# Optimization experiments

Hardware: AMD Instinct MI355X
Metric: run time of the kernel (lower is better)

Reference implementation:

```python
import jax, jax.numpy as jnp
import numpy as np

IN_DIM = 100
OUT_DIM = 200
N_ETYPES = 4
N_STEPS = 8
CONCAT = IN_DIM + OUT_DIM  # 300
EPS = 1e-5


def setup_inputs() -> dict:
    key = jax.random.key(0)
    ks = jax.random.split(key, 24)
    N, E = 100000, 1600000
    rn = lambda k, shape, s=0.05: jax.random.normal(k, shape, dtype=jnp.float32) * s
    return {
        "features": rn(ks[0], (N, IN_DIM), 1.0),
        "edge_index": jax.random.randint(ks[1], (2, E), 0, N, dtype=jnp.int32),
        "edge_types": jax.random.randint(ks[2], (E,), 0, N_ETYPES, dtype=jnp.int32),
        "ggnn_W": rn(ks[3], (N_ETYPES, OUT_DIM, OUT_DIM)),
        "ggnn_b": rn(ks[4], (N_ETYPES, OUT_DIM)),
        "gru_Wih": rn(ks[5], (3 * OUT_DIM, OUT_DIM)),
        "gru_Whh": rn(ks[6], (3 * OUT_DIM, OUT_DIM)),
        "gru_bih": rn(ks[7], (3 * OUT_DIM,)),
        "gru_bhh": rn(ks[8], (3 * OUT_DIM,)),
        "conv1_w": rn(ks[9], (OUT_DIM, OUT_DIM, 3)),
        "conv1_b": rn(ks[10], (OUT_DIM,)),
        "conv2_w": rn(ks[11], (OUT_DIM, OUT_DIM, 1)),
        "conv2_b": rn(ks[12], (OUT_DIM,)),
        "convc1_w": rn(ks[13], (CONCAT, CONCAT, 3)),
        "convc1_b": rn(ks[14], (CONCAT,)),
        "convc2_w": rn(ks[15], (CONCAT, CONCAT, 1)),
        "convc2_b": rn(ks[16], (CONCAT,)),
        "bn_y_g": jnp.ones((OUT_DIM,), jnp.float32),
        "bn_y_b": jnp.zeros((OUT_DIM,), jnp.float32),
        "bn_c_g": jnp.ones((CONCAT,), jnp.float32),
        "bn_c_b": jnp.zeros((CONCAT,), jnp.float32),
        "mlp_y_w": rn(ks[17], (2, OUT_DIM)),
        "mlp_y_b": rn(ks[18], (2,)),
        "mlp_z_w": rn(ks[19], (2, CONCAT)),
        "mlp_z_b": rn(ks[20], (2,)),
    }


def _ggnn(features, src, dst, etypes, W, b, Wih, Whh, bih, bhh):
    """DGL-style GatedGraphConv: per-etype linear, sum-aggregate, GRU update."""
    N = features.shape[0]
    h0 = jnp.concatenate(
        [features, jnp.zeros((N, OUT_DIM - IN_DIM), features.dtype)], axis=-1)

    def step(h, _):
        # transform every node by every etype weight: [n_etypes, N, OUT_DIM]
        t = jnp.einsum('koh,nh->kno', W, h) + b[:, None, :]
        msg = t[etypes, src]                         # [E, OUT_DIM] gather
        a = jax.ops.segment_sum(msg, dst, num_segments=N)  # scatter-add
        # torch GRUCell
        gi = a @ Wih.T + bih
        gh = h @ Whh.T + bhh
        ir, iz, inn = jnp.split(gi, 3, axis=-1)
        hr, hz, hn = jnp.split(gh, 3, axis=-1)
        r = jax.nn.sigmoid(ir + hr)
        z = jax.nn.sigmoid(iz + hz)
        n = jnp.tanh(inn + r * hn)
        return (1.0 - z) * n + z * h, None

    h, _ = jax.lax.scan(step, h0, None, length=N_STEPS)
    return h


def _bn(x, g, b):  # x: [1, C, L], training-mode BatchNorm1d (biased var)
    m = x.mean(axis=(0, 2), keepdims=True)
    v = x.var(axis=(0, 2), keepdims=True)
    return (x - m) * jax.lax.rsqrt(v + EPS) * g[None, :, None] + b[None, :, None]


def _conv1d(x, w, b):  # x: [N, C, L], w: [O, I, k]
    y = jax.lax.conv_general_dilated(
        x, w, window_strides=(1,), padding='VALID',
        dimension_numbers=('NCH', 'OIH', 'NCH'))
    return y + b[None, :, None]


def _maxpool1d(x, k, s):
    return jax.lax.reduce_window(x, -jnp.inf, jax.lax.max,
                                 (1, 1, k), (1, 1, s), 'VALID')


def reference(features, edge_index, edge_types, ggnn_W, ggnn_b,
              gru_Wih, gru_Whh, gru_bih, gru_bhh,
              conv1_w, conv1_b, conv2_w, conv2_b,
              convc1_w, convc1_b, convc2_w, convc2_b,
              bn_y_g, bn_y_b, bn_c_g, bn_c_b,
              mlp_y_w, mlp_y_b, mlp_z_w, mlp_z_b):
    src, dst = edge_index[0], edge_index[1]
    out = _ggnn(features, src, dst, edge_types, ggnn_W, ggnn_b,
                gru_Wih, gru_Whh, gru_bih, gru_bhh)   # [N, 200]
    x_i = features[None]            # [1, N, 100]
    h_i = out[None]                 # [1, N, 200]
    c_i = jnp.concatenate([h_i, x_i], axis=-1)  # [1, N, 300]

    y = _maxpool1d(jax.nn.relu(_bn(_conv1d(jnp.swapaxes(h_i, 1, 2), conv1_w, conv1_b), bn_y_g, bn_y_b)), 3, 2)
    Y2 = jnp.swapaxes(_maxpool1d(jax.nn.relu(_bn(_conv1d(y, conv2_w, conv2_b), bn_y_g, bn_y_b)), 2, 2), 1, 2)

    z = _maxpool1d(jax.nn.relu(_bn(_conv1d(jnp.swapaxes(c_i, 1, 2), convc1_w, convc1_b), bn_c_g, bn_c_b)), 3, 2)
    Z2 = jnp.swapaxes(_maxpool1d(jax.nn.relu(_bn(_conv1d(z, convc2_w, convc2_b), bn_c_g, bn_c_b)), 2, 2), 1, 2)

    before_avg = (Y2 @ mlp_y_w.T + mlp_y_b) * (Z2 @ mlp_z_w.T + mlp_z_b)  # [1, L, 2]
    return jax.nn.sigmoid(before_avg.mean(axis=1))  # [1, 2]
```

## Files before the change

kernel.cpp:

```cpp
#include <hip/hip_runtime.h>
#include <cstddef>
#include <cstdint>


typedef unsigned short u16;
typedef unsigned char u8;
typedef __attribute__((ext_vector_type(8))) short bf16x8;
typedef __attribute__((ext_vector_type(4))) float f32x4;
typedef __attribute__((ext_vector_type(2))) float f32x2;

static __device__ __forceinline__ float bf2f(u16 u) {
  union { unsigned int i; float f; } v; v.i = ((unsigned int)u) << 16; return v.f;
}
static __device__ __forceinline__ u16 f2bf(float f) {
  union { float f; unsigned int i; } v; v.f = f;
  unsigned int r = v.i + 0x7FFFu + ((v.i >> 16) & 1u);
  return (u16)(r >> 16);
}
static __device__ __forceinline__ float sigm(float x) { return 1.f / (1.f + __expf(-x)); }
static __device__ __forceinline__ u8 f2fp8(float x) {
  return (u8)(__builtin_amdgcn_cvt_pk_fp8_f32(x, 0.f, 0, false) & 0xff);
}

static __device__ __forceinline__ void gload16(const void* gp, void* lp) {
  __builtin_amdgcn_global_load_lds(
      (const __attribute__((address_space(1))) void*)gp,
      (__attribute__((address_space(3))) void*)lp, 16, 0, 0);
}

__global__ void fail_k(float* out, float code) { out[0] = code; out[1] = code; }

__global__ void init_hb_k(const float* __restrict__ feat, u16* __restrict__ hb, int N) {
  int total = N * 224;
  for (int i = blockIdx.x * blockDim.x + threadIdx.x; i < total; i += blockDim.x * gridDim.x) {
    int n = i / 224, c = i - n * 224;
    hb[i] = (c < 100) ? f2bf(feat[(size_t)n * 100 + c]) : (u16)0;
  }
}

__global__ void init_hq_k(const float* __restrict__ feat, u8* __restrict__ hqd,
                          u8* __restrict__ ahq, int N) {
  int total = N * 224;
  for (int i = blockIdx.x * blockDim.x + threadIdx.x; i < total; i += blockDim.x * gridDim.x) {
    int n = i / 224, c = i - n * 224;
    u8 v = (c < 100) ? f2fp8(feat[(size_t)n * 100 + c]) : (u8)0;
    hqd[i] = v;
    ahq[(size_t)n * 448 + 224 + c] = v;
  }
}

__global__ void count_deg_k(const int* __restrict__ dst, const int* __restrict__ et,
                            int* __restrict__ deg_et, int N, int E) {
  for (int e = blockIdx.x * blockDim.x + threadIdx.x; e < E; e += blockDim.x * gridDim.x)
    atomicAdd(&deg_et[et[e] * N + dst[e]], 1);
}

__global__ __launch_bounds__(1024) void bsum_k(const int* __restrict__ cnt,
                                               int* __restrict__ bsum, int L) {
  __shared__ int buf[1024];
  int i = blockIdx.x * 1024 + threadIdx.x;
  buf[threadIdx.x] = (i < L) ? cnt[i] : 0;
  __syncthreads();
  for (int o = 512; o > 0; o >>= 1) {
    if (threadIdx.x < o) buf[threadIdx.x] += buf[threadIdx.x + o];
    __syncthreads();
  }
  if (threadIdx.x == 0) bsum[blockIdx.x] = buf[0];
}

__global__ __launch_bounds__(1024) void scanb_k(int* __restrict__ bsum, int nb) {
  __shared__ int buf[1024];
  int v = (threadIdx.x < nb) ? bsum[threadIdx.x] : 0;
  buf[threadIdx.x] = v;
  __syncthreads();
  for (int o = 1; o < 1024; o <<= 1) {
    int t = (threadIdx.x >= o) ? buf[threadIdx.x - o] : 0;
    __syncthreads();
    buf[threadIdx.x] += t;
    __syncthreads();
  }
  if (threadIdx.x < nb) bsum[threadIdx.x] = buf[threadIdx.x] - v;
}

__global__ __launch_bounds__(1024) void scan_fin_k(const int* __restrict__ cnt,
                                                   const int* __restrict__ bsum,
                                                   int* __restrict__ off, int L) {
  __shared__ int buf[1024];
  int i = blockIdx.x * 1024 + threadIdx.x;
  int v = (i < L) ? cnt[i] : 0;
  buf[threadIdx.x] = v;
  __syncthreads();
  for (int o = 1; o < 1024; o <<= 1) {
    int t = (threadIdx.x >= o) ? buf[threadIdx.x - o] : 0;
    __syncthreads();
    buf[threadIdx.x] += t;
    __syncthreads();
  }
  if (i < L) off[i] = buf[threadIdx.x] - v + bsum[blockIdx.x];
}

__global__ void copy_int_k(const int* __restrict__ a, int* __restrict__ b, int n) {
  for (int i = blockIdx.x * blockDim.x + threadIdx.x; i < n; i += blockDim.x * gridDim.x) b[i] = a[i];
}

__global__ void fill_src_k(const int* __restrict__ src, const int* __restrict__ dst,
                           const int* __restrict__ et, int* __restrict__ cursor,
                           int* __restrict__ esrc, int N, int E) {
  for (int e = blockIdx.x * blockDim.x + threadIdx.x; e < E; e += blockDim.x * gridDim.x) {
    int p = atomicAdd(&cursor[et[e] * N + dst[e]], 1);
    esrc[p] = src[e];
  }
}


__global__ void pack_wcat8_k(const float* __restrict__ W, const float* __restrict__ gb,
                             u8* __restrict__ dst) {
  int total = 200 * 832;
  for (int i = blockIdx.x * blockDim.x + threadIdx.x; i < total; i += blockDim.x * gridDim.x) {
    int o = i / 832, kp = i - o * 832;
    float v = 0.f;
    if (kp < 800) { int k = kp / 200, kk = kp - k * 200; v = W[((size_t)k * 200 + o) * 200 + kk]; }
    else if (kp < 804) v = gb[(kp - 800) * 200 + o];
    dst[i] = f2fp8(v);
  }
}

__global__ void pack_wall8_k(const float* __restrict__ Wih, const float* __restrict__ Whh,
                             u8* __restrict__ dst) {
  int total = 800 * 448;
  for (int i = blockIdx.x * blockDim.x + threadIdx.x; i < total; i += blockDim.x * gridDim.x) {
    int jp = i / 448, kp = i - jp * 448;
    int o = jp >> 2, g = jp & 3;
    float v = 0.f;
    if (g == 0) {
      if (kp < 200) v = Wih[(size_t)o * 200 + kp];
      else if (kp >= 224 && kp < 424) v = Whh[(size_t)o * 200 + (kp - 224)];
    } else if (g == 1) {
      if (kp < 200) v = Wih[(size_t)(200 + o) * 200 + kp];
      else if (kp >= 224 && kp < 424) v = Whh[(size_t)(200 + o) * 200 + (kp - 224)];
    } else if (g == 2) {
      if (kp < 200) v = Wih[(size_t)(400 + o) * 200 + kp];
    } else {
      if (kp >= 224 && kp < 424) v = Whh[(size_t)(400 + o) * 200 + (kp - 224)];
    }
    dst[i] = f2fp8(v);
  }
}

__global__ void ball_i_k(const float* __restrict__ bih, const float* __restrict__ bhh,
                         float* __restrict__ ball) {
  int j = blockIdx.x * blockDim.x + threadIdx.x;
  if (j < 800) {
    int o = j >> 2, g = j & 3;
    float v;
    if (g == 0) v = bih[o] + bhh[o];
    else if (g == 1) v = bih[200 + o] + bhh[200 + o];
    else if (g == 2) v = bih[400 + o];
    else v = bhh[400 + o];
    ball[j] = v;
  }
}

__global__ void pack_lin_b(const float* __restrict__ src, u16* __restrict__ dst,
                           int Nn, int K, int Kp) {
  int total = Nn * Kp;
  for (int i = blockIdx.x * blockDim.x + threadIdx.x; i < total; i += blockDim.x * gridDim.x) {
    int o = i / Kp, kp = i - o * Kp;
    dst[i] = (kp < K) ? f2bf(src[(size_t)o * K + kp]) : (u16)0;
  }
}

__global__ void pack_w1c_k(const float* __restrict__ src, u16* __restrict__ dst) {
  int total = 200 * 1056;
  for (int i = blockIdx.x * blockDim.x + threadIdx.x; i < total; i += blockDim.x * gridDim.x) {
    int o = i / 1056, r = i - o * 1056;
    int t = r / 352, kp = r - t * 352;
    dst[i] = (kp < 200) ? f2bf(src[((size_t)o * 200 + kp) * 3 + t]) : (u16)0;
  }
}

__global__ void pack_wc1_b(const float* __restrict__ src, u16* __restrict__ dst) {
  int total = 300 * 1056;
  for (int i = blockIdx.x * blockDim.x + threadIdx.x; i < total; i += blockDim.x * gridDim.x) {
    int o = i / 1056, r = i - o * 1056;
    int t = r / 352, kp = r - t * 352;
    int ci = (kp < 224) ? (kp < 200 ? kp : -1) : ((kp - 224) < 100 ? 200 + (kp - 224) : -1);
    dst[i] = (ci >= 0) ? f2bf(src[((size_t)o * 300 + ci) * 3 + t]) : (u16)0;
  }
}

__global__ void agg8_k(const int* __restrict__ off_et, const int* __restrict__ deg_et,
                       const int* __restrict__ esrc, const u8* __restrict__ hqd,
                       u8* __restrict__ scat8, int N) {
  int gtid = blockIdx.x * blockDim.x + threadIdx.x;
  int wid = gtid >> 6, lane = threadIdx.x & 63;
  int nw = (blockDim.x * gridDim.x) >> 6;
  int sub = lane >> 4, l = lane & 15;
  for (int n = wid; n < N; n += nw) {
    u8* srow = scat8 + (size_t)n * 832;
    int rs = off_et[(size_t)sub * N + n];
    int d  = deg_et[(size_t)sub * N + n];
    f32x2 a2[8];
#pragma unroll
    for (int j = 0; j < 8; ++j) a2[j] = (f32x2)0.f;
    for (int i = 0; i < d; ++i) {
      if (l < 13) {
        const u8* hr = hqd + (size_t)esrc[rs + i] * 224 + l * 16;
        uint4 v = *reinterpret_cast<const uint4*>(hr);
        a2[0] += __builtin_amdgcn_cvt_pk_f32_fp8(v.x, 0);
        a2[1] += __builtin_amdgcn_cvt_pk_f32_fp8(v.x, 1);
        a2[2] += __builtin_amdgcn_cvt_pk_f32_fp8(v.y, 0);
        a2[3] += __builtin_amdgcn_cvt_pk_f32_fp8(v.y, 1);
        a2[4] += __builtin_amdgcn_cvt_pk_f32_fp8(v.z, 0);
        a2[5] += __builtin_amdgcn_cvt_pk_f32_fp8(v.z, 1);
        a2[6] += __builtin_amdgcn_cvt_pk_f32_fp8(v.w, 0);
        a2[7] += __builtin_amdgcn_cvt_pk_f32_fp8(v.w, 1);
      }
    }
    if (l < 13) {
      int d0, d1;
      d0 = __builtin_amdgcn_cvt_pk_fp8_f32(a2[0][0], a2[0][1], 0, false);
      d0 = __builtin_amdgcn_cvt_pk_fp8_f32(a2[1][0], a2[1][1], d0, true);
      d1 = __builtin_amdgcn_cvt_pk_fp8_f32(a2[2][0], a2[2][1], 0, false);
      d1 = __builtin_amdgcn_cvt_pk_fp8_f32(a2[3][0], a2[3][1], d1, true);
      *reinterpret_cast<uint2*>(srow + sub * 200 + l * 16) = make_uint2(d0, d1);
      if (l < 12) {
        int d2, d3;
        d2 = __builtin_amdgcn_cvt_pk_fp8_f32(a2[4][0], a2[4][1], 0, false);
        d2 = __builtin_amdgcn_cvt_pk_fp8_f32(a2[5][0], a2[5][1], d2, true);
        d3 = __builtin_amdgcn_cvt_pk_fp8_f32(a2[6][0], a2[6][1], 0, false);
        d3 = __builtin_amdgcn_cvt_pk_fp8_f32(a2[7][0], a2[7][1], d3, true);
        *reinterpret_cast<uint2*>(srow + sub * 200 + l * 16 + 8) = make_uint2(d2, d3);
      }
    }
    if (sub == 0 && l == 13) {
      float g0 = (float)deg_et[(size_t)0 * N + n];
      float g1 = (float)deg_et[(size_t)1 * N + n];
      float g2 = (float)deg_et[(size_t)2 * N + n];
      float g3 = (float)deg_et[(size_t)3 * N + n];
      int rr = __builtin_amdgcn_cvt_pk_fp8_f32(g0, g1, 0, false);
      rr = __builtin_amdgcn_cvt_pk_fp8_f32(g2, g3, rr, true);
      *reinterpret_cast<unsigned*>(srow + 800) = (unsigned)rr;
    }
    if (sub == 3 && l >= 1 && l <= 7)
      *reinterpret_cast<unsigned*>(srow + 804 + (l - 1) * 4) = 0;
  }
}

__global__ __launch_bounds__(512, 4) void gemm_a8(
    const u8* __restrict__ A, int lda,
    const u8* __restrict__ B, int ldb,
    u8* __restrict__ Cq, int ldcb, int npad,
    int M, int Nn, int K, int gyr) {
  const int gx = gridDim.x;
  int lin = blockIdx.y * gx + blockIdx.x;
  int k8 = lin & 7, j = lin >> 3;
  int band = gridDim.y >> 3;
  int yy = j / gx, xx = j - yy * gx;
  int by = k8 * band + yy;
  if (by >= gyr) return;
  const int m0 = by * 256, n0 = xx * 128;

  __shared__ __align__(16) u8 As[3 * 8192];
  __shared__ __align__(16) u8 Bs[3 * 4096];
  const int tid = threadIdx.x;
  const int lane = tid & 63;
  const int w = tid >> 6;
  const int wr = w >> 1, wc = w & 1;
  const int fr = lane & 15;
  const int g = lane >> 4;

  const int rowA = tid >> 1;
  const int cA = (tid & 1) ^ ((rowA >> 2) & 1);
  int gaA = m0 + rowA; if (gaA >= M) gaA = M - 1;
  const u8* pa = A + (size_t)gaA * lda + cA * 16;
  u8* lA = &As[(size_t)(w * 64) * 16];
  const int sB = w * 32 + (lane & 31);
  const int rowB = sB >> 1;
  const int cB = (sB & 1) ^ ((rowB >> 2) & 1);
  int gbB = n0 + rowB; if (gbB >= Nn) gbB = Nn - 1;
  const u8* pb = B + (size_t)gbB * ldb + cB * 16;
  u8* lB = &Bs[(size_t)(w * 32) * 16];
  const bool doB = (lane < 32);

  const int rdoff = (((g >> 1) ^ ((fr >> 2) & 1)) << 4) + ((g & 1) << 3);

  f32x4 acc[4][4] = {};
  const int nt = K >> 5;
  const int ABUF = 8192, BBUF = 4096;

  gload16(pa, lA);
  if (doB) gload16(pb, lB);
  pa += 32; pb += 32;
  if (nt > 1) {
    gload16(pa, lA + ABUF);
    if (doB) gload16(pb, lB + BBUF);
    pa += 32; pb += 32;
  }

  for (int t = 0; t < nt; ++t) {
    if (t + 1 < nt) asm volatile("s_waitcnt vmcnt(2)" ::: "memory");
    else            asm volatile("s_waitcnt vmcnt(0)" ::: "memory");
    __builtin_amdgcn_s_barrier();
    if (t + 2 < nt) {
      int bi = (t + 2) % 3;
      gload16(pa, lA + bi * ABUF);
      if (doB) gload16(pb, lB + bi * BBUF);
      pa += 32; pb += 32;
    }
    int ca = (t % 3) * ABUF, cbb = (t % 3) * BBUF;
    long af[4], bfv[4];
#pragma unroll
    for (int i = 0; i < 4; ++i) {
      int row = wr * 64 + i * 16 + fr;
      af[i] = *reinterpret_cast<const long*>(&As[ca + row * 32 + rdoff]);
    }
#pragma unroll
    for (int jj = 0; jj < 4; ++jj) {
      int row = wc * 64 + jj * 16 + fr;
      bfv[jj] = *reinterpret_cast<const long*>(&Bs[cbb + row * 32 + rdoff]);
    }
    __builtin_amdgcn_s_setprio(1);
#pragma unroll
    for (int i = 0; i < 4; ++i)
#pragma unroll
      for (int jj = 0; jj < 4; ++jj)
        acc[i][jj] = __builtin_amdgcn_mfma_f32_16x16x32_fp8_fp8(af[i], bfv[jj], acc[i][jj], 0, 0, 0);
    __builtin_amdgcn_s_setprio(0);
  }

  const int er = (lane >> 4) * 4;
  const int ec = lane & 15;
#pragma unroll
  for (int i = 0; i < 4; ++i) {
#pragma unroll
    for (int jj = 0; jj < 4; ++jj) {
      int n = n0 + wc * 64 + jj * 16 + ec;
#pragma unroll
      for (int r = 0; r < 4; ++r) {
        int m = m0 + wr * 64 + i * 16 + er + r;
        if (m >= M) continue;
        if (n < Nn) Cq[(size_t)m * ldcb + n] = f2fp8(acc[i][jj][r]);
        else if (n < npad) Cq[(size_t)m * ldcb + n] = (u8)0;
      }
    }
  }
}

__global__ __launch_bounds__(512, 4) void gemm_gru8(
    const u8* __restrict__ A, int lda,
    const u8* __restrict__ B, int ldb,
    int M, int K, const float* __restrict__ bias,
    u16* __restrict__ hb, u8* __restrict__ hq, int gyr) {
  const int gx = gridDim.x;
  int lin = blockIdx.y * gx + blockIdx.x;
  int k8 = lin & 7, j = lin >> 3;
  int band = gridDim.y >> 3;
  int yy = j / gx, xx = j - yy * gx;
  int by = k8 * band + yy;
  if (by >= gyr) return;
  const int m0 = by * 256, n0 = xx * 128;
  const int Nn = 800;

  __shared__ __align__(16) u8 SM8[65536];
  u8* As = SM8;
  u8* Bs = SM8 + 24576;
  const int tid = threadIdx.x;
  const int lane = tid & 63;
  const int w = tid >> 6;
  const int wr = w >> 1, wc = w & 1;
  const int fr = lane & 15;
  const int g = lane >> 4;

  const int rowA = tid >> 1;
  const int cA = (tid & 1) ^ ((rowA >> 2) & 1);
  int gaA = m0 + rowA; if (gaA >= M) gaA = M - 1;
  const u8* pa = A + (size_t)gaA * lda + cA * 16;
  u8* lA = &As[(size_t)(w * 64) * 16];
  const int sB = w * 32 + (lane & 31);
  const int rowB = sB >> 1;
  const int cB = (sB & 1) ^ ((rowB >> 2) & 1);
  int gbB = n0 + rowB; if (gbB >= Nn) gbB = Nn - 1;
  const u8* pb = B + (size_t)gbB * ldb + cB * 16;
  u8* lB = &Bs[(size_t)(w * 32) * 16];
  const bool doB = (lane < 32);

  const int rdoff = (((g >> 1) ^ ((fr >> 2) & 1)) << 4) + ((g & 1) << 3);

  f32x4 acc[4][4] = {};
  const int nt = K >> 5;
  const int ABUF = 8192, BBUF = 4096;

  gload16(pa, lA);
  if (doB) gload16(pb, lB);
  pa += 32; pb += 32;
  if (nt > 1) {
    gload16(pa, lA + ABUF);
    if (doB) gload16(pb, lB + BBUF);
    pa += 32; pb += 32;
  }

  for (int t = 0; t < nt; ++t) {
    if (t + 1 < nt) asm volatile("s_waitcnt vmcnt(2)" ::: "memory");
    else            asm volatile("s_waitcnt vmcnt(0)" ::: "memory");
    __builtin_amdgcn_s_barrier();
    if (t + 2 < nt) {
      int bi = (t + 2) % 3;
      gload16(pa, lA + bi * ABUF);
      if (doB) gload16(pb, lB + bi * BBUF);
      pa += 32; pb += 32;
    }
    int ca = (t % 3) * ABUF, cbb = (t % 3) * BBUF;
    long af[4], bfv[4];
#pragma unroll
    for (int i = 0; i < 4; ++i) {
      int row = wr * 64 + i * 16 + fr;
      af[i] = *reinterpret_cast<const long*>(&As[ca + row * 32 + rdoff]);
    }
#pragma unroll
    for (int jj = 0; jj < 4; ++jj) {
      int row = wc * 64 + jj * 16 + fr;
      bfv[jj] = *reinterpret_cast<const long*>(&Bs[cbb + row * 32 + rdoff]);
    }
    __builtin_amdgcn_s_setprio(1);
#pragma unroll
    for (int i = 0; i < 4; ++i)
#pragma unroll
      for (int jj = 0; jj < 4; ++jj)
        acc[i][jj] = __builtin_amdgcn_mfma_f32_16x16x32_fp8_fp8(af[i], bfv[jj], acc[i][jj], 0, 0, 0);
    __builtin_amdgcn_s_setprio(0);
  }

  const int er = (lane >> 4) * 4;
  const int ec = lane & 15;
  __syncthreads();
  float* ep = (float*)(SM8) + (size_t)w * 2048;

  for (int hh = 0; hh < 2; ++hh) {
#pragma unroll
    for (int jj2 = 0; jj2 < 2; ++jj2) {
      int jj = hh * 2 + jj2;
      int n = n0 + wc * 64 + jj * 16 + ec;
      float bv = (n < 800) ? bias[n] : 0.f;
#pragma unroll
      for (int i = 0; i < 4; ++i)
#pragma unroll
        for (int r = 0; r < 4; ++r) {
          int row_loc = i * 16 + er + r;
          ep[row_loc * 32 + jj2 * 16 + ec] = acc[i][jj][r] + bv;
        }
    }
    __syncthreads();
#pragma unroll
    for (int p = 0; p < 8; ++p) {
      int idx = p * 64 + lane;
      int row = idx >> 3, og = idx & 7;
      int n_base = n0 + wc * 64 + hh * 32 + og * 4;
      int m = m0 + wr * 64 + row;
      if (n_base < 800 && m < M) {
        f32x4 gv = *reinterpret_cast<f32x4*>(&ep[row * 32 + og * 4]);
        float rg = sigm(gv[0]);
        float zg = sigm(gv[1]);
        float x = gv[2] + rg * gv[3];
        float e2 = __expf(2.f * x);
        float nn = (e2 - 1.f) / (e2 + 1.f);
        int o = n_base >> 2;
        float hold = bf2f(hb[(size_t)m * 224 + o]);
        float hv = (1.f - zg) * nn + zg * hold;
        hb[(size_t)m * 224 + o] = f2bf(hv);
        hq[(size_t)m * 224 + o] = f2fp8(hv);
      }
    }
    __syncthreads();
  }
}

__global__ void hcopy8_k(const u8* __restrict__ hq, u8* __restrict__ ahq, int N) {
  int total = N * 50;
  for (int i = blockIdx.x * blockDim.x + threadIdx.x; i < total; i += blockDim.x * gridDim.x) {
    int n = i / 50, o4 = (i - n * 50) * 4;
    *reinterpret_cast<unsigned*>(ahq + (size_t)n * 448 + 224 + o4) =
        *reinterpret_cast<const unsigned*>(hq + (size_t)n * 224 + o4);
  }
}

__global__ __launch_bounds__(512, 4) void gemm_mfma(
    const u16* __restrict__ A, int lda,
    const u16* __restrict__ B, int ldb,
    u16* __restrict__ Cb, int ldcb, int npad,
    int M, int Nn, int K, const float* __restrict__ bias, int gyr) {
  const int gx = gridDim.x;
  int lin = blockIdx.y * gx + blockIdx.x;
  int k8 = lin & 7, j = lin >> 3;
  int band = gridDim.y >> 3;
  int yy = j / gx, xx = j - yy * gx;
  int by = k8 * band + yy;
  if (by >= gyr) return;
  const int m0 = by * 256, n0 = xx * 128;

  __shared__ __align__(16) u16 As[3 * 8192];
  __shared__ __align__(16) u16 Bs[3 * 4096];
  const int tid = threadIdx.x;
  const int lane = tid & 63;
  const int w = tid >> 6;
  const int wr = w >> 1, wc = w & 1;
  const int fr = lane & 15;
  const int g = lane >> 4;

  const int sA0 = w * 64 + lane, sA1 = sA0 + 512, sB = sA0;
  int rA0 = sA0 >> 2, cA0 = (sA0 & 3) ^ ((rA0 >> 1) & 3);
  int rA1 = sA1 >> 2, cA1 = (sA1 & 3) ^ ((rA1 >> 1) & 3);
  int rB  = sB  >> 2, cB  = (sB & 3) ^ ((rB >> 1) & 3);
  int ga0 = m0 + rA0; if (ga0 >= M) ga0 = M - 1;
  int ga1 = m0 + rA1; if (ga1 >= M) ga1 = M - 1;
  int gb  = n0 + rB;  if (gb >= Nn) gb = Nn - 1;
  const u16* pa0 = A + (size_t)ga0 * lda + cA0 * 8;
  const u16* pa1 = A + (size_t)ga1 * lda + cA1 * 8;
  const u16* pb  = B + (size_t)gb  * ldb + cB * 8;
  u16* lA0 = &As[(w * 64) * 8];
  u16* lA1 = &As[(512 + w * 64) * 8];
  u16* lB  = &Bs[(w * 64) * 8];

  const int gxr = g ^ ((fr >> 1) & 3);

  f32x4 acc[4][4] = {};
  const int nt = K >> 5;
  const int ABUF = 8192, BBUF = 4096;

  gload16(pa0, lA0); gload16(pa1, lA1); gload16(pb, lB);
  pa0 += 32; pa1 += 32; pb += 32;
  if (nt > 1) {
    gload16(pa0, lA0 + ABUF); gload16(pa1, lA1 + ABUF); gload16(pb, lB + BBUF);
    pa0 += 32; pa1 += 32; pb += 32;
  }

  for (int t = 0; t < nt; ++t) {
    if (t + 1 < nt) asm volatile("s_waitcnt vmcnt(3)" ::: "memory");
    else            asm volatile("s_waitcnt vmcnt(0)" ::: "memory");
    __builtin_amdgcn_s_barrier();
    if (t + 2 < nt) {
      int bi = (t + 2) % 3;
      gload16(pa0, lA0 + bi * ABUF); gload16(pa1, lA1 + bi * ABUF); gload16(pb, lB + bi * BBUF);
      pa0 += 32; pa1 += 32; pb += 32;
    }
    int ca = (t % 3) * ABUF, cbb = (t % 3) * BBUF;
    bf16x8 af[4], bfv[4];
#pragma unroll
    for (int i = 0; i < 4; ++i) {
      int row = wr * 64 + i * 16 + fr;
      af[i] = *reinterpret_cast<const bf16x8*>(&As[ca + (row * 4 + gxr) * 8]);
    }
#pragma unroll
    for (int jj = 0; jj < 4; ++jj) {
      int row = wc * 64 + jj * 16 + fr;
      bfv[jj] = *reinterpret_cast<const bf16x8*>(&Bs[cbb + (row * 4 + gxr) * 8]);
    }
    __builtin_amdgcn_s_setprio(1);
#pragma unroll
    for (int i = 0; i < 4; ++i)
#pragma unroll
      for (int jj = 0; jj < 4; ++jj)
        acc[i][jj] = __builtin_amdgcn_mfma_f32_16x16x32_bf16(af[i], bfv[jj], acc[i][jj], 0, 0, 0);
    __builtin_amdgcn_s_setprio(0);
  }

  const int er = (lane >> 4) * 4;
  const int ec = lane & 15;
#pragma unroll
  for (int i = 0; i < 4; ++i) {
#pragma unroll
    for (int jj = 0; jj < 4; ++jj) {
      int n = n0 + wc * 64 + jj * 16 + ec;
#pragma unroll
      for (int r = 0; r < 4; ++r) {
        int m = m0 + wr * 64 + i * 16 + er + r;
        if (m >= M) continue;
        if (n < Nn) {
          float v = acc[i][jj][r];
          if (bias) v += bias[n];
          Cb[(size_t)m * ldcb + n] = f2bf(v);
        } else if (n < npad) {
          Cb[(size_t)m * ldcb + n] = (u16)0;
        }
      }
    }
  }
}

__global__ void cmat_k(const u16* __restrict__ hb, const float* __restrict__ feat,
                       u16* __restrict__ c, int N) {
  int total = N * 352;
  for (int i = blockIdx.x * blockDim.x + threadIdx.x; i < total; i += blockDim.x * gridDim.x) {
    int n = i / 352, j = i - n * 352;
    u16 v;
    if (j < 224) v = hb[(size_t)n * 224 + j];
    else { int f = j - 224; v = (f < 100) ? f2bf(feat[(size_t)n * 100 + f]) : (u16)0; }
    c[i] = v;
  }
}

__global__ __launch_bounds__(1024) void bn_stats2_k(const u16* __restrict__ X, int L, int C,
                                                    float* __restrict__ stats) {
  const int Q = 1024 / C;
  const int T = Q * C;
  const int tid = threadIdx.x;
  float s = 0.f, q = 0.f;
  int c = 0;
  if (tid < T) {
    int qi = tid / C; c = tid - qi * C;
    for (size_t r = (size_t)blockIdx.x * Q + qi; r < (size_t)L; r += (size_t)gridDim.x * Q) {
      float v = bf2f(X[r * C + c]);
      s += v; q += v * v;
    }
  }
  __shared__ float sb[304], qb[304];
  for (int cc = tid; cc < C; cc += 1024) { sb[cc] = 0.f; qb[cc] = 0.f; }
  __syncthreads();
  if (tid < T) { atomicAdd(&sb[c], s); atomicAdd(&qb[c], q); }
  __syncthreads();
  for (int cc = tid; cc < C; cc += 1024) {
    atomicAdd(&stats[cc], sb[cc]);
    atomicAdd(&stats[C + cc], qb[cc]);
  }
}

__global__ void bn_fin_k(const float* __restrict__ stats, const float* __restrict__ g,
                         const float* __restrict__ b, int C, float Linv,
                         float* __restrict__ scsh) {
  int c = blockIdx.x * blockDim.x + threadIdx.x;
  if (c < C) {
    float mean = stats[c] * Linv;
    float var = stats[C + c] * Linv - mean * mean;
    float sc = g[c] * rsqrtf(var + 1e-5f);
    scsh[c] = sc;
    scsh[C + c] = b[c] - mean * sc;
  }
}

__global__ void pool_bf_k(const u16* __restrict__ X, int C, const float* __restrict__ scsh,
                          int kw, int stride, u16* __restrict__ Y, int Cpad, int Lout) {
  int total = Lout * Cpad;
  for (int i = blockIdx.x * blockDim.x + threadIdx.x; i < total; i += blockDim.x * gridDim.x) {
    int lp = i / Cpad, c = i - lp * Cpad;
    if (c >= C) { Y[i] = (u16)0; continue; }
    float sc = scsh[c], sh = scsh[C + c];
    int l0 = lp * stride;
    float m = 0.f;
    for (int wq = 0; wq < kw; ++wq)
      m = fmaxf(m, fmaf(bf2f(X[(size_t)(l0 + wq) * C + c]), sc, sh));
    Y[i] = f2bf(m);
  }
}

__global__ void pool_f32_k(const u16* __restrict__ X, int C, const float* __restrict__ scsh,
                           int kw, int stride, float* __restrict__ Y, int Lout) {
  int total = Lout * C;
  for (int i = blockIdx.x * blockDim.x + threadIdx.x; i < total; i += blockDim.x * gridDim.x) {
    int lp = i / C, c = i - lp * C;
    float sc = scsh[c], sh = scsh[C + c];
    int l0 = lp * stride;
    float m = 0.f;
    for (int wq = 0; wq < kw; ++wq)
      m = fmaxf(m, fmaf(bf2f(X[(size_t)(l0 + wq) * C + c]), sc, sh));
    Y[i] = m;
  }
}

__global__ __launch_bounds__(256) void final_dot_k(
    const float* __restrict__ Y2, const float* __restrict__ Z2,
    const float* __restrict__ wy, const float* __restrict__ by,
    const float* __restrict__ wz, const float* __restrict__ bz,
    float* __restrict__ acc, int L) {
  float s0 = 0.f, s1 = 0.f;
  for (int lp = blockIdx.x * blockDim.x + threadIdx.x; lp < L; lp += blockDim.x * gridDim.x) {
    const float* y = Y2 + (size_t)lp * 200;
    const float* z = Z2 + (size_t)lp * 300;
    float d0 = 0.f, d1 = 0.f;
    for (int k = 0; k < 200; ++k) { float v = y[k]; d0 += v * wy[k]; d1 += v * wy[200 + k]; }
    float e0 = 0.f, e1 = 0.f;
    for (int k = 0; k < 300; ++k) { float v = z[k]; e0 += v * wz[k]; e1 += v * wz[300 + k]; }
    s0 += (d0 + by[0]) * (e0 + bz[0]);
    s1 += (d1 + by[1]) * (e1 + bz[1]);
  }
  __shared__ float r0[256], r1[256];
  r0[threadIdx.x] = s0; r1[threadIdx.x] = s1;
  __syncthreads();
  for (int off = 128; off > 0; off >>= 1) {
    if (threadIdx.x < off) { r0[threadIdx.x] += r0[threadIdx.x + off]; r1[threadIdx.x] += r1[threadIdx.x + off]; }
    __syncthreads();
  }
  if (threadIdx.x == 0) { atomicAdd(&acc[0], r0[0]); atomicAdd(&acc[1], r1[0]); }
}

__global__ void final_out_k(const float* __restrict__ acc, float invL, float* __restrict__ out) {
  int j = threadIdx.x;
  if (j < 2) out[j] = 1.f / (1.f + expf(-acc[j] * invL));
}


static inline void gemmL(hipStream_t st, const u16* A, int lda, const u16* B, int ldb,
                         u16* Cb, int ldcb, int npad, int M, int Nn, int K, const float* bias) {
  int ncols = (npad > Nn) ? npad : Nn;
  int gx = (ncols + 127) / 128;
  int gy = (M + 255) / 256;
  int gyp = ((gy + 7) / 8) * 8;
  dim3 g(gx, gyp);
  gemm_mfma<<<g, 512, 0, st>>>(A, lda, B, ldb, Cb, ldcb, npad, M, Nn, K, bias, gy);
}

extern "C" void kernel_launch(void* const* d_in, const int* in_sizes, int n_in,
                              void* d_out, int out_size, void* d_ws, size_t ws_size,
                              hipStream_t stream) {
  (void)n_in; (void)out_size;
  const float* feat    = (const float*)d_in[0];
  const int*   eix     = (const int*)d_in[1];
  const int*   etyp    = (const int*)d_in[2];
  const float* ggnnW   = (const float*)d_in[3];
  const float* ggnnB   = (const float*)d_in[4];
  const float* Wih     = (const float*)d_in[5];
  const float* Whh     = (const float*)d_in[6];
  const float* bih     = (const float*)d_in[7];
  const float* bhh     = (const float*)d_in[8];
  const float* conv1w  = (const float*)d_in[9];
  const float* conv2w  = (const float*)d_in[11];
  const float* convc1w = (const float*)d_in[13];
  const float* convc2w = (const float*)d_in[15];
  const float* bnyg    = (const float*)d_in[17];
  const float* bnyb    = (const float*)d_in[18];
  const float* bncg    = (const float*)d_in[19];
  const float* bncb    = (const float*)d_in[20];
  const float* mlpyw   = (const float*)d_in[21];
  const float* mlpyb   = (const float*)d_in[22];
  const float* mlpzw   = (const float*)d_in[23];
  const float* mlpzb   = (const float*)d_in[24];

  const int N = in_sizes[0] / 100;
  const int E = in_sizes[2];
  const int* src = eix;
  const int* dst = eix + E;

  char* base = (char*)d_ws;
  const size_t AHQ_B = (size_t)N * 448;
  const size_t HB_B  = (size_t)N * 224 * 2;
  const size_t HQD_B = (size_t)N * 224;
  const int CH = (N + 1) / 2;
  const size_t SCR_B = (size_t)CH * 1664;

  u8*  ahq = (u8*)base;
  u16* hb  = (u16*)(base + AHQ_B);
  u8*  hqd = (u8*)(base + AHQ_B + HB_B);
  char* R1 = base + AHQ_B + HB_B + HQD_B;
  char* WREG = R1 + SCR_B;

  u8*  Wcat8 = (u8*)WREG;
  u8*  Wall8 = Wcat8 + 166400;
  u16* w1c   = (u16*)(Wall8 + 358400);
  u16* c2b   = w1c + 211200;
  u16* wc1   = c2b + 44800;
  u16* wc2   = wc1 + 316800;
  float* ball  = (float*)(wc2 + 96000);
  float* stats = ball + 832;
  float* scsh  = stats + 600;
  float* acc2  = scsh + 600;
  int* deg_et = (int*)(acc2 + 8);
  int* off_et = deg_et + 4 * (size_t)N;
  int* cursor = off_et + 4 * (size_t)N;
  int* esrc   = cursor + 4 * (size_t)N;
  int* bsum   = esrc + E;
  const int L4 = 4 * N;
  const int NB = (L4 + 1023) / 1024;
  size_t need = (size_t)((char*)(bsum + NB) - base);

  if (ws_size < need) {
    fail_k<<<1, 64, 0, stream>>>((float*)d_out, -(float)(ws_size >> 20));
    return;
  }

  hipMemsetAsync(deg_et, 0, sizeof(int) * 4 * (size_t)N, stream);
  init_hb_k<<<2048, 256, 0, stream>>>(feat, hb, N);
  init_hq_k<<<2048, 256, 0, stream>>>(feat, hqd, ahq, N);
  count_deg_k<<<2048, 256, 0, stream>>>(dst, etyp, deg_et, N, E);
  bsum_k<<<NB, 1024, 0, stream>>>(deg_et, bsum, L4);
  scanb_k<<<1, 1024, 0, stream>>>(bsum, NB);
  scan_fin_k<<<NB, 1024, 0, stream>>>(deg_et, bsum, off_et, L4);
  copy_int_k<<<512, 256, 0, stream>>>(off_et, cursor, L4);
  fill_src_k<<<2048, 256, 0, stream>>>(src, dst, etyp, cursor, esrc, N, E);
  pack_wcat8_k<<<651, 256, 0, stream>>>(ggnnW, ggnnB, Wcat8);
  pack_wall8_k<<<1400, 256, 0, stream>>>(Wih, Whh, Wall8);
  ball_i_k<<<4, 256, 0, stream>>>(bih, bhh, ball);
  pack_w1c_k<<<825, 256, 0, stream>>>(conv1w, w1c);
  pack_lin_b<<<175, 256, 0, stream>>>(conv2w, c2b, 200, 200, 224);
  pack_wc1_b<<<1238, 256, 0, stream>>>(convc1w, wc1);
  pack_lin_b<<<375, 256, 0, stream>>>(convc2w, wc2, 300, 300, 320);

  u8* scat8 = (u8*)R1;

  const int gy = (N + 255) / 256;
  const int gyp = ((gy + 7) / 8) * 8;

  for (int step = 0; step < 8; ++step) {
    agg8_k<<<4096, 256, 0, stream>>>(off_et, deg_et, esrc, hqd, scat8, N);
    gemm_a8<<<dim3(2, gyp), 512, 0, stream>>>(scat8, 832, Wcat8, 832,
                                              ahq, 448, 224, N, 200, 832, gy);
    gemm_gru8<<<dim3(7, gyp), 512, 0, stream>>>(ahq, 448, Wall8, 448, N, 448, ball,
                                                hb, hqd, gy);
    hcopy8_k<<<2048, 256, 0, stream>>>(hqd, ahq, N);
  }

  const int L1 = N - 2;
  const int L2 = (L1 - 3) / 2 + 1;
  const int L3 = (L2 - 2) / 2 + 1;

  u16* cmat = (u16*)R1;
  u16* out1 = (u16*)base;
  size_t y1_off = (((size_t)L1 * 400) + 255) & ~(size_t)255;
  u16* y1 = (u16*)(base + y1_off);
  size_t o2_off = y1_off + ((((size_t)L2 * 448) + 255) & ~(size_t)255);
  u16* out2 = (u16*)(base + o2_off);
  float* Y2f = (float*)base;
  size_t oc1_off = (((size_t)L3 * 800) + 255) & ~(size_t)255;
  u16* outc1 = (u16*)(base + oc1_off);
  u16* z1 = (u16*)R1;
  size_t oc2_off = (((size_t)L2 * 640) + 255) & ~(size_t)255;
  u16* outc2 = (u16*)(R1 + oc2_off);
  float* Z2f = (float*)(base + oc1_off);

  cmat_k<<<4096, 256, 0, stream>>>(hb, feat, cmat, N);

  gemmL(stream, cmat, 352, w1c, 1056, out1, 200, 200, L1, 200, 1056, nullptr);
  hipMemsetAsync(stats, 0, sizeof(float) * 400, stream);
  bn_stats2_k<<<512, 1024, 0, stream>>>(out1, L1, 200, stats);
  bn_fin_k<<<2, 256, 0, stream>>>(stats, bnyg, bnyb, 200, 1.f / (float)L1, scsh);
  pool_bf_k<<<2048, 256, 0, stream>>>(out1, 200, scsh, 3, 2, y1, 224, L2);

  gemmL(stream, y1, 224, c2b, 224, out2, 200, 200, L2, 200, 224, nullptr);
  hipMemsetAsync(stats, 0, sizeof(float) * 400, stream);
  bn_stats2_k<<<512, 1024, 0, stream>>>(out2, L2, 200, stats);
  bn_fin_k<<<2, 256, 0, stream>>>(stats, bnyg, bnyb, 200, 1.f / (float)L2, scsh);
  pool_f32_k<<<2048, 256, 0, stream>>>(out2, 200, scsh, 2, 2, Y2f, L3);

  gemmL(stream, cmat, 352, wc1, 1056, outc1, 300, 300, L1, 300, 1056, nullptr);
  hipMemsetAsync(stats, 0, sizeof(float) * 600, stream);
  bn_stats2_k<<<512, 1024, 0, stream>>>(outc1, L1, 300, stats);
  bn_fin_k<<<2, 256, 0, stream>>>(stats, bncg, bncb, 300, 1.f / (float)L1, scsh);
  pool_bf_k<<<2048, 256, 0, stream>>>(outc1, 300, scsh, 3, 2, z1, 320, L2);

  gemmL(stream, z1, 320, wc2, 320, outc2, 300, 300, L2, 300, 320, nullptr);
  hipMemsetAsync(stats, 0, sizeof(float) * 600, stream);
  bn_stats2_k<<<512, 1024, 0, stream>>>(outc2, L2, 300, stats);
  bn_fin_k<<<2, 256, 0, stream>>>(stats, bncg, bncb, 300, 1.f / (float)L2, scsh);
  pool_f32_k<<<2048, 256, 0, stream>>>(outc2, 300, scsh, 2, 2, Z2f, L3);

  hipMemsetAsync(acc2, 0, sizeof(float) * 2, stream);
  final_dot_k<<<256, 256, 0, stream>>>(Y2f, Z2f, mlpyw, mlpyb, mlpzw, mlpzb, acc2, L3);
  final_out_k<<<1, 64, 0, stream>>>(acc2, 1.f / (float)L3, (float*)d_out);
}
```

Measured before the change: 2.985 ms.

## Ping-pong fp8 hidden state and read two A sources in GRU GEMM

Drops the per-step hcopy8 kernel that copied the fp8 hidden state into the concatenated [a|h] buffer. The GRU GEMM now takes two separate A pointers (aggregate and previous hidden state) and switches source halfway through K, while the hidden state ping-pongs between two buffers. The change also software-prefetches the next gathered row in the aggregation loop and pads the epilogue LDS stride from 32 to 36 floats to reduce bank conflicts, which grows shared memory from 64 KB to 72 KB and may lower occupancy.

```diff
diff --git a/kernel.cpp b/kernel.cpp
--- a/kernel.cpp
+++ b/kernel.cpp
@@ -38,14 +38,11 @@
   }
 }
 
-__global__ void init_hq_k(const float* __restrict__ feat, u8* __restrict__ hqd,
-                          u8* __restrict__ ahq, int N) {
+__global__ void init_hq_k(const float* __restrict__ feat, u8* __restrict__ hq0, int N) {
   int total = N * 224;
   for (int i = blockIdx.x * blockDim.x + threadIdx.x; i < total; i += blockDim.x * gridDim.x) {
     int n = i / 224, c = i - n * 224;
-    u8 v = (c < 100) ? f2fp8(feat[(size_t)n * 100 + c]) : (u8)0;
-    hqd[i] = v;
-    ahq[(size_t)n * 448 + 224 + c] = v;
+    hq0[i] = (c < 100) ? f2fp8(feat[(size_t)n * 100 + c]) : (u8)0;
   }
 }
 
@@ -203,10 +200,11 @@
     f32x2 a2[8];
 #pragma unroll
     for (int j = 0; j < 8; ++j) a2[j] = (f32x2)0.f;
-    for (int i = 0; i < d; ++i) {
-      if (l < 13) {
-        const u8* hr = hqd + (size_t)esrc[rs + i] * 224 + l * 16;
-        uint4 v = *reinterpret_cast<const uint4*>(hr);
+    if (l < 13 && d > 0) {
+      const size_t lo = (size_t)l * 16;
+      uint4 v = *reinterpret_cast<const uint4*>(hqd + (size_t)esrc[rs] * 224 + lo);
+      for (int i = 1; i < d; ++i) {
+        uint4 vn = *reinterpret_cast<const uint4*>(hqd + (size_t)esrc[rs + i] * 224 + lo);
         a2[0] += __builtin_amdgcn_cvt_pk_f32_fp8(v.x, 0);
         a2[1] += __builtin_amdgcn_cvt_pk_f32_fp8(v.x, 1);
         a2[2] += __builtin_amdgcn_cvt_pk_f32_fp8(v.y, 0);
@@ -215,7 +213,16 @@
         a2[5] += __builtin_amdgcn_cvt_pk_f32_fp8(v.z, 1);
         a2[6] += __builtin_amdgcn_cvt_pk_f32_fp8(v.w, 0);
         a2[7] += __builtin_amdgcn_cvt_pk_f32_fp8(v.w, 1);
+        v = vn;
       }
+      a2[0] += __builtin_amdgcn_cvt_pk_f32_fp8(v.x, 0);
+      a2[1] += __builtin_amdgcn_cvt_pk_f32_fp8(v.x, 1);
+      a2[2] += __builtin_amdgcn_cvt_pk_f32_fp8(v.y, 0);
+      a2[3] += __builtin_amdgcn_cvt_pk_f32_fp8(v.y, 1);
+      a2[4] += __builtin_amdgcn_cvt_pk_f32_fp8(v.z, 0);
+      a2[5] += __builtin_amdgcn_cvt_pk_f32_fp8(v.z, 1);
+      a2[6] += __builtin_amdgcn_cvt_pk_f32_fp8(v.w, 0);
+      a2[7] += __builtin_amdgcn_cvt_pk_f32_fp8(v.w, 1);
     }
     if (l < 13) {
       int d0, d1;
@@ -348,10 +355,10 @@
 }
 
 __global__ __launch_bounds__(512, 4) void gemm_gru8(
-    const u8* __restrict__ A, int lda,
+    const u8* __restrict__ Aa, const u8* __restrict__ Ah,
     const u8* __restrict__ B, int ldb,
-    int M, int K, const float* __restrict__ bias,
-    u16* __restrict__ hb, u8* __restrict__ hq, int gyr) {
+    int M, const float* __restrict__ bias,
+    u16* __restrict__ hb, u8* __restrict__ hqout, int gyr) {
   const int gx = gridDim.x;
   int lin = blockIdx.y * gx + blockIdx.x;
   int k8 = lin & 7, j = lin >> 3;
@@ -362,7 +369,7 @@
   const int m0 = by * 256, n0 = xx * 128;
   const int Nn = 800;
 
-  __shared__ __align__(16) u8 SM8[65536];
+  __shared__ __align__(16) u8 SM8[73728];
   u8* As = SM8;
   u8* Bs = SM8 + 24576;
   const int tid = threadIdx.x;
@@ -375,7 +382,8 @@
   const int rowA = tid >> 1;
   const int cA = (tid & 1) ^ ((rowA >> 2) & 1);
   int gaA = m0 + rowA; if (gaA >= M) gaA = M - 1;
-  const u8* pa = A + (size_t)gaA * lda + cA * 16;
+  const u8* paA = Aa + (size_t)gaA * 224 + cA * 16;
+  const u8* paH = Ah + (size_t)gaA * 224 + cA * 16;
   u8* lA = &As[(size_t)(w * 64) * 16];
   const int sB = w * 32 + (lane & 31);
   const int rowB = sB >> 1;
@@ -388,27 +396,27 @@
   const int rdoff = (((g >> 1) ^ ((fr >> 2) & 1)) << 4) + ((g & 1) << 3);
 
   f32x4 acc[4][4] = {};
-  const int nt = K >> 5;
+  const int nt = 14, kh = 7;
   const int ABUF = 8192, BBUF = 4096;
 
-  gload16(pa, lA);
+  gload16(paA, lA);
   if (doB) gload16(pb, lB);
-  pa += 32; pb += 32;
-  if (nt > 1) {
-    gload16(pa, lA + ABUF);
-    if (doB) gload16(pb, lB + BBUF);
-    pa += 32; pb += 32;
-  }
+  pb += 32;
+  gload16(paA + 32, lA + ABUF);
+  if (doB) gload16(pb, lB + BBUF);
+  pb += 32;
 
   for (int t = 0; t < nt; ++t) {
     if (t + 1 < nt) asm volatile("s_waitcnt vmcnt(2)" ::: "memory");
     else            asm volatile("s_waitcnt vmcnt(0)" ::: "memory");
     __builtin_amdgcn_s_barrier();
-    if (t + 2 < nt) {
-      int bi = (t + 2) % 3;
-      gload16(pa, lA + bi * ABUF);
+    int tt = t + 2;
+    if (tt < nt) {
+      int bi = tt % 3;
+      const u8* srcA = (tt < kh) ? (paA + tt * 32) : (paH + (tt - kh) * 32);
+      gload16(srcA, lA + bi * ABUF);
       if (doB) gload16(pb, lB + bi * BBUF);
-      pa += 32; pb += 32;
+      pb += 32;
     }
     int ca = (t % 3) * ABUF, cbb = (t % 3) * BBUF;
     long af[4], bfv[4];
@@ -434,7 +442,7 @@
   const int er = (lane >> 4) * 4;
   const int ec = lane & 15;
   __syncthreads();
-  float* ep = (float*)(SM8) + (size_t)w * 2048;
+  float* ep = (float*)(SM8) + (size_t)w * 2304;
 
   for (int hh = 0; hh < 2; ++hh) {
 #pragma unroll
@@ -447,7 +455,7 @@
 #pragma unroll
         for (int r = 0; r < 4; ++r) {
           int row_loc = i * 16 + er + r;
-          ep[row_loc * 32 + jj2 * 16 + ec] = acc[i][jj][r] + bv;
+          ep[row_loc * 36 + jj2 * 16 + ec] = acc[i][jj][r] + bv;
         }
     }
     __syncthreads();
@@ -458,7 +466,7 @@
       int n_base = n0 + wc * 64 + hh * 32 + og * 4;
       int m = m0 + wr * 64 + row;
       if (n_base < 800 && m < M) {
-        f32x4 gv = *reinterpret_cast<f32x4*>(&ep[row * 32 + og * 4]);
+        f32x4 gv = *reinterpret_cast<f32x4*>(&ep[row * 36 + og * 4]);
         float rg = sigm(gv[0]);
         float zg = sigm(gv[1]);
         float x = gv[2] + rg * gv[3];
@@ -468,19 +476,10 @@
         float hold = bf2f(hb[(size_t)m * 224 + o]);
         float hv = (1.f - zg) * nn + zg * hold;
         hb[(size_t)m * 224 + o] = f2bf(hv);
-        hq[(size_t)m * 224 + o] = f2fp8(hv);
+        hqout[(size_t)m * 224 + o] = f2fp8(hv);
       }
     }
     __syncthreads();
-  }
-}
-
-__global__ void hcopy8_k(const u8* __restrict__ hq, u8* __restrict__ ahq, int N) {
-  int total = N * 50;
-  for (int i = blockIdx.x * blockDim.x + threadIdx.x; i < total; i += blockDim.x * gridDim.x) {
-    int n = i / 50, o4 = (i - n * 50) * 4;
-    *reinterpret_cast<unsigned*>(ahq + (size_t)n * 448 + 224 + o4) =
-        *reinterpret_cast<const unsigned*>(hq + (size_t)n * 224 + o4);
   }
 }
 
@@ -740,16 +739,16 @@
   const int* dst = eix + E;
 
   char* base = (char*)d_ws;
-  const size_t AHQ_B = (size_t)N * 448;
   const size_t HB_B  = (size_t)N * 224 * 2;
-  const size_t HQD_B = (size_t)N * 224;
+  const size_t Q_B   = (size_t)N * 224;
   const int CH = (N + 1) / 2;
   const size_t SCR_B = (size_t)CH * 1664;
 
-  u8*  ahq = (u8*)base;
-  u16* hb  = (u16*)(base + AHQ_B);
-  u8*  hqd = (u8*)(base + AHQ_B + HB_B);
-  char* R1 = base + AHQ_B + HB_B + HQD_B;
+  u16* hb  = (u16*)base;
+  u8*  aq  = (u8*)(base + HB_B);
+  u8*  hq0 = aq + Q_B;
+  u8*  hq1 = hq0 + Q_B;
+  char* R1 = (char*)(hq1 + Q_B);
   char* WREG = R1 + SCR_B;
 
   u8*  Wcat8 = (u8*)WREG;
@@ -778,7 +777,7 @@
 
   hipMemsetAsync(deg_et, 0, sizeof(int) * 4 * (size_t)N, stream);
   init_hb_k<<<2048, 256, 0, stream>>>(feat, hb, N);
-  init_hq_k<<<2048, 256, 0, stream>>>(feat, hqd, ahq, N);
+  init_hq_k<<<2048, 256, 0, stream>>>(feat, hq0, N);
   count_deg_k<<<2048, 256, 0, stream>>>(dst, etyp, deg_et, N, E);
   bsum_k<<<NB, 1024, 0, stream>>>(deg_et, bsum, L4);
   scanb_k<<<1, 1024, 0, stream>>>(bsum, NB);
@@ -798,13 +797,15 @@
   const int gy = (N + 255) / 256;
   const int gyp = ((gy + 7) / 8) * 8;
 
+  u8* hqA = hq0;
+  u8* hqB = hq1;
   for (int step = 0; step < 8; ++step) {
-    agg8_k<<<4096, 256, 0, stream>>>(off_et, deg_et, esrc, hqd, scat8, N);
+    agg8_k<<<4096, 256, 0, stream>>>(off_et, deg_et, esrc, hqA, scat8, N);
     gemm_a8<<<dim3(2, gyp), 512, 0, stream>>>(scat8, 832, Wcat8, 832,
-                                              ahq, 448, 224, N, 200, 832, gy);
-    gemm_gru8<<<dim3(7, gyp), 512, 0, stream>>>(ahq, 448, Wall8, 448, N, 448, ball,
-                                                hb, hqd, gy);
-    hcopy8_k<<<2048, 256, 0, stream>>>(hqd, ahq, N);
+                                              aq, 224, 224, N, 200, 832, gy);
+    gemm_gru8<<<dim3(7, gyp), 512, 0, stream>>>(aq, hqA, Wall8, 448, N, ball,
+                                                hb, hqB, gy);
+    u8* t = hqA; hqA = hqB; hqB = t;
   }
 
   const int L1 = N - 2;
```

Result: faster. 2.859 ms (-4.2%).
